# Optimization experiments

Hardware: AMD Instinct MI355X
Metric: run time of the kernel (lower is better)

## Reference

```python
import jax, jax.numpy as jnp
import numpy as np

BINS = 10


def setup_inputs() -> dict:
    key = jax.random.key(0)
    k1, k2 = jax.random.split(key)
    N, C = 4194304, 16
    inputs = jax.random.normal(k1, (N, C), dtype=jnp.float32)
    target = jax.random.randint(k2, (N,), 0, 2, dtype=jnp.int64)
    return {"inputs": inputs, "target": target}


def reference(inputs, target):
    N = inputs.shape[0]
    edges = jnp.arange(BINS + 1, dtype=inputs.dtype) / BINS  # [0, 0.1, ..., 1.0]

    # p_t = softmax(inputs)[i, target_i]
    logp = jax.nn.log_softmax(inputs, axis=1)
    p_t = jnp.take_along_axis(jnp.exp(logp), target[:, None], axis=1)[:, 0]

    # gradient norm g = |p_t - target| (detached in the original)
    g = jnp.abs(jax.lax.stop_gradient(p_t) - target.astype(inputs.dtype))

    # bin index: matches (g >= edges[i]) & (g < edges[i+1]); clip handles g == 1.0
    bin_idx = jnp.clip(jnp.searchsorted(edges, g, side="right") - 1, 0, BINS - 1)

    # per-bin counts via one scatter-add (replaces the per-bin CPU loop)
    counts = jax.ops.segment_sum(jnp.ones_like(g), bin_idx, num_segments=BINS)
    counts = jnp.maximum(counts, 1.0)  # occupied bins always have count >= 1

    # weights[i] = (N / bins) / num_in_bin(i)
    weights = (N / BINS) / counts[bin_idx]

    # weighted cross entropy, summed
    nll = -jnp.take_along_axis(logp, target[:, None], axis=1)[:, 0]
    return jnp.sum(nll * weights)
```

## Files before the change

kernel.cpp:

```cpp
#include <hip/hip_runtime.h>

#define BINS 10
#define GRID 2048
#define BLOCK 256
#define NWAVES (BLOCK / 64)

__global__ __launch_bounds__(BLOCK) void ghm_main(const float* __restrict__ x,
                                                  const int* __restrict__ tgt,
                                                  float* __restrict__ p_sum,
                                                  unsigned int* __restrict__ p_cnt,
                                                  int n_rows) {
    float h_sum[BINS];
    unsigned int h_cnt[BINS];
    #pragma unroll
    for (int b = 0; b < BINS; ++b) { h_sum[b] = 0.0f; h_cnt[b] = 0u; }

    const int lane = threadIdx.x & 63;
    const int j = threadIdx.x & 3;
    const int quad0 = (blockIdx.x * BLOCK + threadIdx.x) >> 2;
    const int quads_total = (GRID * BLOCK) >> 2;
    const float4* __restrict__ xv = (const float4*)x;

    const float edges[BINS] = {0.1f, 0.2f, 0.3f, 0.4f, 0.5f,
                               0.6f, 0.7f, 0.8f, 0.9f, 1.0f};

    for (int r = quad0; r < n_rows; r += quads_total) {
        const float4 v = xv[(size_t)r * 4 + j];
        const int tg = tgt[r];

        const int c = tg & 3;
        const float cand = (c < 2) ? ((c == 0) ? v.x : v.y) : ((c == 2) ? v.z : v.w);
        const float xt = __shfl(cand, (lane & 60) + (tg >> 2));

        float s = __expf(v.x - xt) + __expf(v.y - xt) + __expf(v.z - xt) + __expf(v.w - xt);
        s += __shfl_xor(s, 1);
        s += __shfl_xor(s, 2);

        if (j == 0) {
            const float nll = __logf(s);
            const float g = fabsf(1.0f / s - (float)tg);

            int b = 0;
            #pragma unroll
            for (int k = 0; k < BINS; ++k) b += (g >= edges[k]) ? 1 : 0;
            b = (b > BINS - 1) ? (BINS - 1) : b;

            #pragma unroll
            for (int k = 0; k < BINS; ++k) {
                if (b == k) { h_sum[k] += nll; h_cnt[k] += 1u; }
            }
        }
    }

    __shared__ float ls[NWAVES * BINS];
    __shared__ unsigned int lc[NWAVES * BINS];
    const int wv = threadIdx.x >> 6;
    #pragma unroll
    for (int b = 0; b < BINS; ++b) {
        float s = h_sum[b];
        unsigned int cn = h_cnt[b];
        #pragma unroll
        for (int off = 32; off > 0; off >>= 1) {
            s += __shfl_xor(s, off);
            cn += __shfl_xor(cn, off);
        }
        if (lane == 0) { ls[wv * BINS + b] = s; lc[wv * BINS + b] = cn; }
    }
    __syncthreads();

    if (threadIdx.x < BINS) {
        float s = 0.0f;
        unsigned int cn = 0u;
        #pragma unroll
        for (int w = 0; w < NWAVES; ++w) { s += ls[w * BINS + threadIdx.x]; cn += lc[w * BINS + threadIdx.x]; }
        p_sum[threadIdx.x * GRID + blockIdx.x] = s;
        p_cnt[threadIdx.x * GRID + blockIdx.x] = cn;
    }
}

__global__ void ghm_final(const float* __restrict__ p_sum,
                          const unsigned int* __restrict__ p_cnt,
                          float* __restrict__ out, int n_rows) {
    const int lane = threadIdx.x;
    double total = 0.0;
    for (int b = 0; b < BINS; ++b) {
        double s = 0.0;
        unsigned long long c = 0;
        for (int k = lane; k < GRID; k += 64) {
            s += (double)p_sum[b * GRID + k];
            c += (unsigned long long)p_cnt[b * GRID + k];
        }
        #pragma unroll
        for (int off = 32; off > 0; off >>= 1) {
            s += __shfl_xor(s, off);
            c += __shfl_xor(c, off);
        }
        double cd = (double)c;
        if (cd < 1.0) cd = 1.0;
        total += s / cd;
    }
    if (lane == 0) out[0] = (float)(total * ((double)n_rows / (double)BINS));
}

extern "C" void kernel_launch(void* const* d_in, const int* in_sizes, int n_in,
                              void* d_out, int out_size, void* d_ws, size_t ws_size,
                              hipStream_t stream) {
    const float* x = (const float*)d_in[0];
    const int* tgt = (const int*)d_in[1];
    const int n_rows = in_sizes[1];

    float* p_sum = (float*)d_ws;
    unsigned int* p_cnt = (unsigned int*)((char*)d_ws + BINS * GRID * sizeof(float));

    ghm_main<<<GRID, BLOCK, 0, stream>>>(x, tgt, p_sum, p_cnt, n_rows);
    ghm_final<<<1, 64, 0, stream>>>(p_sum, p_cnt, (float*)d_out, n_rows);
}
```

Baseline: 452.8 us.

## Unroll grid-stride loop by two and accumulate bins with LDS atomics

Processes two rows per thread per iteration so two float4 loads and target loads are in flight together, raising memory-level parallelism. Per-thread register histograms and the end-of-block shuffle reductions are replaced by shared-memory atomicAdd into per-wave bin arrays. This frees registers but adds LDS atomic contention, since many lanes of a wave hit the same few bins. The loop drops the bounds check on the second row, so it relies on n_rows being a multiple of twice the stride, which holds for the test size.

```diff
diff --git a/kernel.cpp b/kernel.cpp
--- a/kernel.cpp
+++ b/kernel.cpp
@@ -10,61 +10,64 @@
                                                   float* __restrict__ p_sum,
                                                   unsigned int* __restrict__ p_cnt,
                                                   int n_rows) {
-    float h_sum[BINS];
-    unsigned int h_cnt[BINS];
-    #pragma unroll
-    for (int b = 0; b < BINS; ++b) { h_sum[b] = 0.0f; h_cnt[b] = 0u; }
+    __shared__ float ws_sum[NWAVES][BINS];
+    __shared__ unsigned int ws_cnt[NWAVES][BINS];
 
     const int lane = threadIdx.x & 63;
+    const int wv = threadIdx.x >> 6;
+    if (lane < BINS) { ws_sum[wv][lane] = 0.0f; ws_cnt[wv][lane] = 0u; }
+
     const int j = threadIdx.x & 3;
     const int quad0 = (blockIdx.x * BLOCK + threadIdx.x) >> 2;
-    const int quads_total = (GRID * BLOCK) >> 2;
+    const int qstride = (GRID * BLOCK) >> 2;
     const float4* __restrict__ xv = (const float4*)x;
 
     const float edges[BINS] = {0.1f, 0.2f, 0.3f, 0.4f, 0.5f,
                                0.6f, 0.7f, 0.8f, 0.9f, 1.0f};
 
-    for (int r = quad0; r < n_rows; r += quads_total) {
-        const float4 v = xv[(size_t)r * 4 + j];
-        const int tg = tgt[r];
+    for (int r = quad0; r < n_rows; r += 2 * qstride) {
+        const int r2 = r + qstride;
+        const float4 va = xv[(size_t)r * 4 + j];
+        const float4 vb = xv[(size_t)r2 * 4 + j];
+        const int ta = tgt[r];
+        const int tb = tgt[r2];
 
-        const int c = tg & 3;
-        const float cand = (c < 2) ? ((c == 0) ? v.x : v.y) : ((c == 2) ? v.z : v.w);
-        const float xt = __shfl(cand, (lane & 60) + (tg >> 2));
-
-        float s = __expf(v.x - xt) + __expf(v.y - xt) + __expf(v.z - xt) + __expf(v.w - xt);
-        s += __shfl_xor(s, 1);
-        s += __shfl_xor(s, 2);
-
-        if (j == 0) {
-            const float nll = __logf(s);
-            const float g = fabsf(1.0f / s - (float)tg);
-
-            int b = 0;
-            #pragma unroll
-            for (int k = 0; k < BINS; ++k) b += (g >= edges[k]) ? 1 : 0;
-            b = (b > BINS - 1) ? (BINS - 1) : b;
-
-            #pragma unroll
-            for (int k = 0; k < BINS; ++k) {
-                if (b == k) { h_sum[k] += nll; h_cnt[k] += 1u; }
+        {
+            const int c = ta & 3;
+            const float cand = (c < 2) ? ((c == 0) ? va.x : va.y) : ((c == 2) ? va.z : va.w);
+            const float xt = __shfl(cand, (lane & 60) + (ta >> 2));
+            float s = __expf(va.x - xt) + __expf(va.y - xt) + __expf(va.z - xt) + __expf(va.w - xt);
+            s += __shfl_xor(s, 1);
+            s += __shfl_xor(s, 2);
+            if (j == 0) {
+                const float nll = __logf(s);
+                const float g = fabsf(1.0f / s - (float)ta);
+                int b = 0;
+                #pragma unroll
+                for (int k = 0; k < BINS; ++k) b += (g >= edges[k]) ? 1 : 0;
+                b = (b > BINS - 1) ? (BINS - 1) : b;
+                atomicAdd(&ws_sum[wv][b], nll);
+                atomicAdd(&ws_cnt[wv][b], 1u);
             }
         }
-    }
-
-    __shared__ float ls[NWAVES * BINS];
-    __shared__ unsigned int lc[NWAVES * BINS];
-    const int wv = threadIdx.x >> 6;
-    #pragma unroll
-    for (int b = 0; b < BINS; ++b) {
-        float s = h_sum[b];
-        unsigned int cn = h_cnt[b];
-        #pragma unroll
-        for (int off = 32; off > 0; off >>= 1) {
-            s += __shfl_xor(s, off);
-            cn += __shfl_xor(cn, off);
+        {
+            const int c = tb & 3;
+            const float cand = (c < 2) ? ((c == 0) ? vb.x : vb.y) : ((c == 2) ? vb.z : vb.w);
+            const float xt = __shfl(cand, (lane & 60) + (tb >> 2));
+            float s = __expf(vb.x - xt) + __expf(vb.y - xt) + __expf(vb.z - xt) + __expf(vb.w - xt);
+            s += __shfl_xor(s, 1);
+            s += __shfl_xor(s, 2);
+            if (j == 0) {
+                const float nll = __logf(s);
+                const float g = fabsf(1.0f / s - (float)tb);
+                int b = 0;
+                #pragma unroll
+                for (int k = 0; k < BINS; ++k) b += (g >= edges[k]) ? 1 : 0;
+                b = (b > BINS - 1) ? (BINS - 1) : b;
+                atomicAdd(&ws_sum[wv][b], nll);
+                atomicAdd(&ws_cnt[wv][b], 1u);
+            }
         }
-        if (lane == 0) { ls[wv * BINS + b] = s; lc[wv * BINS + b] = cn; }
     }
     __syncthreads();
 
@@ -72,7 +75,7 @@
         float s = 0.0f;
         unsigned int cn = 0u;
         #pragma unroll
-        for (int w = 0; w < NWAVES; ++w) { s += ls[w * BINS + threadIdx.x]; cn += lc[w * BINS + threadIdx.x]; }
+        for (int w = 0; w < NWAVES; ++w) { s += ws_sum[w][threadIdx.x]; cn += ws_cnt[w][threadIdx.x]; }
         p_sum[threadIdx.x * GRID + blockIdx.x] = s;
         p_cnt[threadIdx.x * GRID + blockIdx.x] = cn;
     }
```

Result: no change. 455.9 us (+0.7%).
